# Kernel optimization log

Measured on AMD Instinct MI355X. Metric: run time of the kernel, lower is better.

## Reference

```python
import jax, jax.numpy as jnp
import numpy as np
import math

B, H, W, DM = 4, 64, 64, 96
DS, DCONV, EXPAND = 16, 3, 2
DI = EXPAND * DM
DTR = math.ceil(DM / 16)
K = 4
HID = 4 * DI


def layernorm(x, g, b, eps=1e-5):
    m = x.mean(-1, keepdims=True)
    v = ((x - m) ** 2).mean(-1, keepdims=True)
    return (x - m) / jnp.sqrt(v + eps) * g + b


def dwconv(x, w, b=None):
    # x: (B,C,H,W), w: (C,1,kh,kw) depthwise, odd kernel => SAME padding == k//2
    out = jax.lax.conv_general_dilated(x, w, (1, 1), 'SAME',
                                       feature_group_count=x.shape[1],
                                       dimension_numbers=('NCHW', 'OIHW', 'NCHW'))
    if b is not None:
        out = out + b[None, :, None, None]
    return out


def ss2d_core(xc, x_proj_w, dt_projs_w, dt_projs_b, A_logs, Ds):
    # xc: (b, d_inner, h, w) -> (b, d_inner, L) summed over 4 scan directions
    b, c, h, w = xc.shape
    L = h * w
    x_hw = xc.reshape(b, c, L)
    x_wh = xc.transpose(0, 1, 3, 2).reshape(b, c, L)
    xs = jnp.stack([x_hw, x_wh], axis=1)                 # (b,2,c,L)
    xs = jnp.concatenate([xs, jnp.flip(xs, -1)], axis=1)  # (b,4,c,L)
    x_dbl = jnp.einsum('bkdl,kcd->bkcl', xs, x_proj_w)
    dts, Bs, Cs = jnp.split(x_dbl, [DTR, DTR + DS], axis=2)
    dts = jnp.einsum('bkrl,kdr->bkdl', dts, dt_projs_w)
    delta = jax.nn.softplus(dts + dt_projs_b[None, :, :, None])  # (b,K,c,L)
    A = -jnp.exp(A_logs).reshape(K, c, DS)                       # (K,c,n)

    def step(hst, inp):
        x_t, d_t, B_t, C_t = inp  # (b,K,c),(b,K,c),(b,K,n),(b,K,n)
        dA = jnp.exp(d_t[..., None] * A)                       # (b,K,c,n)
        hst = hst * dA + (d_t * x_t)[..., None] * B_t[:, :, None, :]
        y = jnp.einsum('bkdn,bkn->bkd', hst, C_t)
        return hst, y

    seq = (jnp.moveaxis(xs, -1, 0), jnp.moveaxis(delta, -1, 0),
           jnp.moveaxis(Bs, -1, 0), jnp.moveaxis(Cs, -1, 0))
    h0 = jnp.zeros((b, K, c, DS), xc.dtype)
    _, ys = jax.lax.scan(step, h0, seq)          # (L,b,K,c)
    ys = jnp.moveaxis(ys, 0, -1)                 # (b,K,c,L)
    ys = ys + Ds.reshape(K, c)[None, :, :, None] * xs
    y1 = ys[:, 0]
    inv = jnp.flip(ys[:, 2:4], -1)
    y2 = inv[:, 0]
    wh = ys[:, 1].reshape(b, c, w, h).swapaxes(2, 3).reshape(b, c, L)
    invwh = inv[:, 1].reshape(b, c, w, h).swapaxes(2, 3).reshape(b, c, L)
    return y1 + y2 + wh + invwh


def msffn(y, in_w, in_b, dw1, dw3, dw5, ln_g, ln_b, out_w, out_b):
    hcl = jax.nn.silu(y @ in_w.T + in_b)          # (b,h,w,HID)
    hc = hcl.transpose(0, 3, 1, 2)
    hc = hc + dwconv(hc, dw1) + dwconv(hc, dw3) + dwconv(hc, dw5)
    hn = layernorm(hc.transpose(0, 2, 3, 1), ln_g, ln_b)
    return hn @ out_w.T + out_b


def setup_inputs() -> dict:
    key = jax.random.key(0)
    ks = jax.random.split(key, 16)
    dt_init_std = DTR ** -0.5
    dt = jnp.exp(jax.random.uniform(ks[0], (K, DI)) * (math.log(0.1) - math.log(0.001)) + math.log(0.001))
    dt = jnp.clip(dt, 1e-4, None)
    inv_dt = dt + jnp.log(-jnp.expm1(-dt))          # softplus-inverse init for dt bias
    A_logs = jnp.tile(jnp.log(jnp.arange(1, DS + 1, dtype=jnp.float32))[None, :], (K * DI, 1))
    r = lambda i, sh, s: jax.random.normal(ks[i], sh, jnp.float32) * s
    return {
        'x': r(1, (B, H, W, DM), 1.0),
        'in_proj_w': r(2, (2 * DI, DM), DM ** -0.5),
        'conv_w': r(3, (DI, 1, DCONV, DCONV), 0.2),
        'conv_b': jnp.zeros((DI,), jnp.float32),
        'x_proj_w': r(4, (K, DTR + 2 * DS, DI), DI ** -0.5),
        'dt_projs_w': jax.random.uniform(ks[5], (K, DI, DTR), minval=-dt_init_std, maxval=dt_init_std),
        'dt_projs_b': inv_dt,
        'A_logs': A_logs,
        'Ds': jnp.ones((K * DI,), jnp.float32),
        'out_norm_g': jnp.ones((DI,), jnp.float32),
        'out_norm_b': jnp.zeros((DI,), jnp.float32),
        'out_proj_w': r(6, (DM, DI), DI ** -0.5),
        'ffn_in_w': r(7, (HID, DI), DI ** -0.5),
        'ffn_in_b': jnp.zeros((HID,), jnp.float32),
        'ffn_dw1': r(8, (HID, 1, 1, 1), 0.3),
        'ffn_dw3': r(9, (HID, 1, 3, 3), 0.2),
        'ffn_dw5': r(10, (HID, 1, 5, 5), 0.1),
        'ffn_ln_g': jnp.ones((HID,), jnp.float32),
        'ffn_ln_b': jnp.zeros((HID,), jnp.float32),
        'ffn_out_w': r(11, (DM, HID), HID ** -0.5),
        'ffn_out_b': jnp.zeros((DM,), jnp.float32),
        'skip_scale': jnp.ones((1,), jnp.float32),
    }


def reference(x, in_proj_w, conv_w, conv_b, x_proj_w, dt_projs_w, dt_projs_b, A_logs, Ds,
              out_norm_g, out_norm_b, out_proj_w, ffn_in_w, ffn_in_b, ffn_dw1, ffn_dw3,
              ffn_dw5, ffn_ln_g, ffn_ln_b, ffn_out_w, ffn_out_b, skip_scale):
    b, h, w, _ = x.shape
    xz = x @ in_proj_w.T                          # (b,h,w,2*DI)
    xi, z = jnp.split(xz, 2, axis=-1)
    xc = jax.nn.silu(dwconv(xi.transpose(0, 3, 1, 2), conv_w, conv_b))  # (b,DI,h,w)
    y = ss2d_core(xc, x_proj_w, dt_projs_w, dt_projs_b, A_logs, Ds)     # (b,DI,L)
    y = y.swapaxes(1, 2).reshape(b, h, w, DI)
    y = layernorm(y, out_norm_g, out_norm_b)
    y = y * jax.nn.silu(z)
    out = y @ out_proj_w.T
    ffn = msffn(y, ffn_in_w, ffn_in_b, ffn_dw1, ffn_dw3, ffn_dw5,
                ffn_ln_g, ffn_ln_b, ffn_out_w, ffn_out_b)
    return out + skip_scale * ffn
```

## Files before the change

### kernel.cpp

```cpp
#include <hip/hip_runtime.h>
#include <hip/hip_bf16.h>

constexpr int BB = 4, HH = 64, WW = 64, DMv = 96;
constexpr int DSn = 16, DIv = 192, DTRv = 6, KKv = 4, HIDv = 768;
constexpr int LL = 4096;
constexpr int NC = 64, CHK = LL / NC;
constexpr int NR = BB * LL;
constexpr int XDS = 40;

constexpr size_t S_xi   = (size_t)BB * LL * DIv;
constexpr size_t S_xdbl = (size_t)BB * KKv * LL * XDS;
constexpr size_t S_big  = (size_t)BB * KKv * LL * DIv;
constexpr size_t S_sp   = (size_t)BB * KKv * NC * DIv * DSn;

typedef __attribute__((ext_vector_type(8))) short short8;
typedef __attribute__((ext_vector_type(4))) short short4v;
typedef __attribute__((ext_vector_type(4))) float floatx4;

__device__ __forceinline__ float sigf(float x) { return 1.f / (1.f + __expf(-x)); }
__device__ __forceinline__ float softp(float x) {
  return (x > 20.f) ? x : __logf(1.f + __expf(x));
}
__device__ __forceinline__ short bfbits(float v) {
  __hip_bfloat16 h = __float2bfloat16(v);
  return *(short*)&h;
}

__device__ __forceinline__ int lmap(int k, int l) {
  int lr = (k & 2) ? (LL - 1 - l) : l;
  return (k & 1) ? (((lr & 63) << 6) | (lr >> 6)) : lr;
}

__global__ void k_wprep(const float* __restrict__ fiw, const float* __restrict__ opw,
                        const float* __restrict__ fow, const float* __restrict__ in_w,
                        const float* __restrict__ xpw, const float* __restrict__ x,
                        float* __restrict__ wt, float* __restrict__ wcatT,
                        float* __restrict__ xt, short* __restrict__ fiwP,
                        short* __restrict__ opwP, short* __restrict__ fowP) {
  int bx = blockIdx.x, t = threadIdx.x;
  __shared__ float smbuf[32 * 65];
  if (bx < 36) {
    int r0 = (bx / 3) * 32, c0 = (bx % 3) * 32;
    float (*tile)[33] = (float(*)[33])smbuf;
    int tc = t & 31, tr = t >> 5;
#pragma unroll
    for (int i = 0; i < 4; ++i)
      tile[tr + i * 8][tc] = in_w[(size_t)(r0 + tr + i * 8) * 96 + c0 + tc];
    __syncthreads();
#pragma unroll
    for (int i = 0; i < 4; ++i)
      wt[(size_t)(c0 + tr + i * 8) * 384 + r0 + tc] = tile[tc][tr + i * 8];
    return;
  }
  if (bx < 150) {
    int idx = (bx - 36) * 256 + t;
    if (idx < 2 * 192 * 76) {
      int p = idx / (192 * 76);
      int rem = idx % (192 * 76);
      int d = rem / 76, j = rem % 76;
      int k = (j >= 38 ? 2 : 0) + p;
      int c = (j >= 38) ? j - 38 : j;
      wcatT[idx] = xpw[((size_t)(k * 38 + c)) * DIv + d];
    }
    return;
  }
  if (bx < 918) {
    int i4 = bx - 150;
    int r0 = (i4 / 3) * 64, k0 = (i4 % 3) * 32;
    float (*tile)[65] = (float(*)[65])smbuf;
#pragma unroll
    for (int ii = 0; ii < 8; ++ii) {
      int i = (t >> 5) + ii * 8, j = t & 31;
      tile[j][i] = x[(size_t)(r0 + i) * 96 + k0 + j];
    }
    __syncthreads();
#pragma unroll
    for (int jj = 0; jj < 8; ++jj) {
      int j = (t >> 6) + jj * 4, i = t & 63;
      xt[(size_t)(k0 + j) * NR + r0 + i] = tile[j][i];
    }
    return;
  }
  int lane = t & 63, ln16 = lane & 15, qd = lane >> 4;
  if (bx < 990) {
    int f = (bx - 918) * 4 + (t >> 6);
    int kt = f / 48, ntg = f % 48;
    int n = ntg * 16 + ln16;
#pragma unroll
    for (int j = 0; j < 8; ++j) {
      int k = kt * 32 + qd * 8 + j;
      fiwP[(size_t)f * 512 + lane * 8 + j] = bfbits(fiw[(size_t)n * DIv + k]);
    }
    return;
  }
  if (bx < 1008) {
    int u = (bx - 990) * 4 + (t >> 6);
    int f = u >> 1, part = u & 1;
    int kt = f / 6, ntg = f % 6;
    int n = ntg * 16 + ln16;
#pragma unroll
    for (int j = 0; j < 8; ++j) {
      int k = kt * 32 + qd * 8 + j;
      float w = opw[(size_t)n * DIv + k];
      __hip_bfloat16 h = __float2bfloat16(w);
      float v = part ? (w - (float)h) : w;
      opwP[((size_t)(part * 36 + f)) * 512 + lane * 8 + j] = bfbits(v);
    }
    return;
  }
  {
    int u = (bx - 1008) * 4 + (t >> 6);
    int f = u >> 1, part = u & 1;
    int kt = f / 6, ntg = f % 6;
    int n = ntg * 16 + ln16;
#pragma unroll
    for (int j = 0; j < 8; ++j) {
      int k = kt * 32 + qd * 8 + j;
      float w = fow[(size_t)n * HIDv + k];
      __hip_bfloat16 h = __float2bfloat16(w);
      float v = part ? (w - (float)h) : w;
      fowP[((size_t)(part * 144 + f)) * 512 + lane * 8 + j] = bfbits(v);
    }
  }
}

__global__ void k_inproj(const float* __restrict__ xt, const float* __restrict__ wt,
                         float* __restrict__ xi, float* __restrict__ z) {
  int t = threadIdx.x;
  int wv = t >> 6, lane = t & 63;
  int rq = blockIdx.x * 256 + wv * 64 + lane;
  int c0 = blockIdx.y * 8;
  const float4* xt4 = (const float4*)xt;
  float4 acc[8];
#pragma unroll
  for (int c = 0; c < 8; ++c) acc[c] = make_float4(0.f, 0.f, 0.f, 0.f);
  for (int k = 0; k < 96; ++k) {
    float4 xv = xt4[(size_t)k * (NR / 4) + rq];
    const float* wr = wt + k * 384 + c0;
#pragma unroll
    for (int c = 0; c < 8; ++c) {
      float w = wr[c];
      acc[c].x += w * xv.x; acc[c].y += w * xv.y;
      acc[c].z += w * xv.z; acc[c].w += w * xv.w;
    }
  }
  float* dst; int cc;
  if (c0 < DIv) { dst = xi; cc = c0; } else { dst = z; cc = c0 - DIv; }
#pragma unroll
  for (int li = 0; li < 4; ++li) {
    size_t row = (size_t)rq * 4 + li;
    float4 v0, v1;
    v0.x = (&acc[0].x)[li]; v0.y = (&acc[1].x)[li];
    v0.z = (&acc[2].x)[li]; v0.w = (&acc[3].x)[li];
    v1.x = (&acc[4].x)[li]; v1.y = (&acc[5].x)[li];
    v1.z = (&acc[6].x)[li]; v1.w = (&acc[7].x)[li];
    float4* o4 = (float4*)(dst + row * DIv + cc);
    o4[0] = v0; o4[1] = v1;
  }
}

constexpr int TW2 = 18;
__global__ void k_dwconv3(const float* __restrict__ xi, const float* __restrict__ cw,
                          const float* __restrict__ cb, float* __restrict__ xc,
                          float* __restrict__ xcT, float* __restrict__ xcTs) {
  int tile = blockIdx.x;
  int cg = blockIdx.y, b = blockIdx.z;
  int t = threadIdx.x;
  int ti0 = (tile >> 2) * 16, tj0 = (tile & 3) * 16;
  __shared__ float sm[TW2 * TW2 * 32];

  for (int e = t; e < TW2 * TW2 * 32; e += 256) {
    int ec = e & 31;
    int sp = e >> 5;
    int hi = sp / TW2, hj = sp % TW2;
    int gi = ti0 + hi - 1, gj = tj0 + hj - 1;
    float v = 0.f;
    if ((unsigned)gi < (unsigned)HH && (unsigned)gj < (unsigned)WW)
      v = xi[((size_t)b * LL + gi * WW + gj) * DIv + cg * 32 + ec];
    sm[e] = v;
  }

  int c = t & 31, s0 = t >> 5;
  int cglob = cg * 32 + c;
  float wc[9];
#pragma unroll
  for (int j = 0; j < 9; ++j) wc[j] = cw[cglob * 9 + j];
  float bv = cb[cglob];
  __syncthreads();

  float res[32];
  for (int i = 0; i < 32; ++i) {
    int p = s0 + (i << 3);
    int r = p >> 4, q = p & 15;
    float s = bv;
#pragma unroll
    for (int di = 0; di < 3; ++di)
#pragma unroll
      for (int dj = 0; dj < 3; ++dj)
        s += sm[((r + di) * TW2 + (q + dj)) * 32 + c] * wc[di * 3 + dj];
    res[i] = s * sigf(s);
  }
  __syncthreads();
  for (int i = 0; i < 32; ++i) {
    int p = s0 + (i << 3);
    sm[p * 35 + c] = res[i];
  }
  __syncthreads();
  for (int it = 0; it < 32; ++it) {
    int e = it * 256 + t;
    int p = e >> 5, ec = e & 31;
    int l = (ti0 + (p >> 4)) * WW + tj0 + (p & 15);
    xc[((size_t)b * LL + l) * DIv + cg * 32 + ec] = sm[p * 35 + ec];
  }
  for (int d2 = 0; d2 < 32; ++d2) {
    int l = (ti0 + (t >> 4)) * WW + tj0 + (t & 15);
    xcT[(size_t)(cg * 32 + d2) * NR + b * LL + l] = sm[t * 35 + d2];
  }
  for (int d2 = 0; d2 < 32; ++d2) {
    int gjo = t >> 4, gio = t & 15;
    int lt2 = (tj0 + gjo) * WW + ti0 + gio;
    int p = gio * 16 + gjo;
    xcTs[(size_t)(cg * 32 + d2) * NR + b * LL + lt2] = sm[p * 35 + d2];
  }
}

__global__ void k_xdbl2(const float* __restrict__ xcT, const float* __restrict__ xcTs,
                        const float* __restrict__ wcatT, float* __restrict__ xdbl) {
  int t = threadIdx.x;
  int rq = blockIdx.x * 256 + t;
  int jg = blockIdx.y;
  int pb = blockIdx.z;
  int p = pb >> 2, b = pb & 3;
  const float4* A = (const float4*)(p ? xcTs : xcT);
  const float* wbase = wcatT + (size_t)p * 192 * 76 + jg * 4;
  float4 acc[4];
#pragma unroll
  for (int j = 0; j < 4; ++j) acc[j] = make_float4(0.f, 0.f, 0.f, 0.f);
  for (int d = 0; d < 192; ++d) {
    float4 xv = A[(size_t)d * (NR / 4) + b * 1024 + rq];
    const float* wr = wbase + d * 76;
#pragma unroll
    for (int j = 0; j < 4; ++j) {
      float w = wr[j];
      acc[j].x += w * xv.x; acc[j].y += w * xv.y;
      acc[j].z += w * xv.z; acc[j].w += w * xv.w;
    }
  }
#pragma unroll
  for (int li = 0; li < 4; ++li) {
    int r = rq * 4 + li;
#pragma unroll
    for (int j = 0; j < 4; ++j) {
      int col = jg * 4 + j;
      int kk = (col >= 38) ? (2 + p) : p;
      int c = (col >= 38) ? col - 38 : col;
      int l = (col >= 38) ? (LL - 1 - r) : r;
      int phys = c + (c >= 6 ? 2 : 0);
      size_t ro = (((size_t)(b * KKv + kk)) * LL + l) * XDS;
      xdbl[ro + phys] = (&acc[j].x)[li];
      if (col == 5) { xdbl[ro + 6] = 0.f; xdbl[ro + 7] = 0.f; }
    }
  }
}

__global__ void k_scan1(const float* __restrict__ xdbl, const float* __restrict__ xc,
                        const float* __restrict__ alogs, const float* __restrict__ dtw,
                        const float* __restrict__ dtb,
                        float* __restrict__ S, float* __restrict__ P) {
  int bx = blockIdx.x;
  int c = bx / 3, dblk = bx % 3;
  int k = blockIdx.y, b = blockIdx.z;
  int t = threadIdx.x, dl = t >> 2, nq = t & 3;
  int d = dblk * 64 + dl;
  __shared__ float de_s[16][64], xv_s[16][64], bc_s[16][16];
  float A[4];
#pragma unroll
  for (int j = 0; j < 4; ++j)
    A[j] = -__expf(alogs[(size_t)(k * DIv + d) * DSn + nq * 4 + j]);
  int derow = t >> 4, dec0 = (t & 15) * 4;
  float DTW[4][6], DTB[4];
#pragma unroll
  for (int jj = 0; jj < 4; ++jj) {
    int dd = k * DIv + dblk * 64 + dec0 + jj;
    DTB[jj] = dtb[dd];
#pragma unroll
    for (int r2 = 0; r2 < 6; ++r2) DTW[jj][r2] = dtw[(size_t)dd * 6 + r2];
  }
  size_t bkL = (size_t)(b * KKv + k) * LL;
  const float* xq = xdbl + bkL * XDS;
  const float* xcb = xc + (size_t)b * LL * DIv;
  float h[4] = {0.f, 0.f, 0.f, 0.f}, sA[4] = {0.f, 0.f, 0.f, 0.f};
  int l0 = c * CHK;
  for (int tile = 0; tile < CHK / 16; ++tile) {
    int lt = l0 + tile * 16;
    __syncthreads();
    {
      int r = t >> 4, q = t & 15;
      int lc = lmap(k, lt + r);
      *(float4*)&xv_s[r][q * 4] = *(const float4*)(xcb + (size_t)lc * DIv + dblk * 64 + q * 4);
      if (t < 64) {
        int r2 = t >> 2, q2 = t & 3;
        *(float4*)&bc_s[r2][q2 * 4] = *(const float4*)(xq + (size_t)(lt + r2) * XDS + 8 + q2 * 4);
      }
      const float* dtp = xq + (size_t)(lt + derow) * XDS;
      float d0 = dtp[0], d1 = dtp[1], d2 = dtp[2], d3 = dtp[3], d4 = dtp[4], d5 = dtp[5];
#pragma unroll
      for (int jj = 0; jj < 4; ++jj) {
        float s = DTB[jj] + d0 * DTW[jj][0] + d1 * DTW[jj][1] + d2 * DTW[jj][2]
                          + d3 * DTW[jj][3] + d4 * DTW[jj][4] + d5 * DTW[jj][5];
        de_s[derow][dec0 + jj] = softp(s);
      }
    }
    __syncthreads();
#pragma unroll
    for (int i2 = 0; i2 < 16; ++i2) {
      float de = de_s[i2][dl];
      float xv = xv_s[i2][dl];
      float4 Bv = *(float4*)&bc_s[i2][nq * 4];
      float db = de * xv;
#pragma unroll
      for (int j = 0; j < 4; ++j) {
        float u = de * A[j];
        sA[j] += u;
        h[j] = h[j] * __expf(u) + db * (&Bv.x)[j];
      }
    }
  }
  size_t o = ((((size_t)(b * KKv + k) * NC + c) * 3 + dblk) * 1024) + (size_t)t * 4;
  float4 hs, ps;
#pragma unroll
  for (int j = 0; j < 4; ++j) { (&hs.x)[j] = h[j]; (&ps.x)[j] = __expf(sA[j]); }
  *(float4*)(S + o) = hs;
  *(float4*)(P + o) = ps;
}

__global__ void k_scan2(float* __restrict__ S, const float* __restrict__ P) {
  int dblk = blockIdx.x, k = blockIdx.y, b = blockIdx.z;
  int t = threadIdx.x;
  size_t base = (((size_t)(b * KKv + k) * NC) * 3 + dblk) * 1024 + (size_t)t * 4;
  float4 h = make_float4(0.f, 0.f, 0.f, 0.f);
  for (int c = 0; c < NC; ++c) {
    size_t o = base + (size_t)c * 3 * 1024;
    float4 s = *(float4*)(S + o), p = *(float4*)(P + o);
    *(float4*)(S + o) = h;
    h.x = s.x + p.x * h.x; h.y = s.y + p.y * h.y;
    h.z = s.z + p.z * h.z; h.w = s.w + p.w * h.w;
  }
}

__global__ void k_scan3(const float* __restrict__ xdbl, const float* __restrict__ xc,
                        const float* __restrict__ alogs, const float* __restrict__ dtw,
                        const float* __restrict__ dtb,
                        const float* __restrict__ Hin, float* __restrict__ ys) {
  int bx = blockIdx.x;
  int c = bx / 3, dblk = bx % 3;
  int k = blockIdx.y, b = blockIdx.z;
  int t = threadIdx.x, dl = t >> 2, nq = t & 3;
  int d = dblk * 64 + dl;
  __shared__ float de_s[16][64], xv_s[16][64], bc_s[16][32];
  float A[4];
#pragma unroll
  for (int j = 0; j < 4; ++j)
    A[j] = -__expf(alogs[(size_t)(k * DIv + d) * DSn + nq * 4 + j]);
  int derow = t >> 4, dec0 = (t & 15) * 4;
  float DTW[4][6], DTB[4];
#pragma unroll
  for (int jj = 0; jj < 4; ++jj) {
    int dd = k * DIv + dblk * 64 + dec0 + jj;
    DTB[jj] = dtb[dd];
#pragma unroll
    for (int r2 = 0; r2 < 6; ++r2) DTW[jj][r2] = dtw[(size_t)dd * 6 + r2];
  }
  size_t bkL = (size_t)(b * KKv + k) * LL;
  const float* xq = xdbl + bkL * XDS;
  const float* xcb = xc + (size_t)b * LL * DIv;
  float* yp = ys + bkL * DIv + d;
  size_t o = ((((size_t)(b * KKv + k) * NC + c) * 3 + dblk) * 1024) + (size_t)t * 4;
  float4 h4 = *(const float4*)(Hin + o);
  float h[4] = {h4.x, h4.y, h4.z, h4.w};
  int l0 = c * CHK;
  for (int tile = 0; tile < CHK / 16; ++tile) {
    int lt = l0 + tile * 16;
    __syncthreads();
    {
      int r = t >> 4, q = t & 15;
      int lc = lmap(k, lt + r);
      *(float4*)&xv_s[r][q * 4] = *(const float4*)(xcb + (size_t)lc * DIv + dblk * 64 + q * 4);
      if (t < 128) {
        int r2 = t >> 3, q2 = t & 7;
        *(float4*)&bc_s[r2][q2 * 4] = *(const float4*)(xq + (size_t)(lt + r2) * XDS + 8 + q2 * 4);
      }
      const float* dtp = xq + (size_t)(lt + derow) * XDS;
      float d0 = dtp[0], d1 = dtp[1], d2 = dtp[2], d3 = dtp[3], d4 = dtp[4], d5 = dtp[5];
#pragma unroll
      for (int jj = 0; jj < 4; ++jj) {
        float s = DTB[jj] + d0 * DTW[jj][0] + d1 * DTW[jj][1] + d2 * DTW[jj][2]
                          + d3 * DTW[jj][3] + d4 * DTW[jj][4] + d5 * DTW[jj][5];
        de_s[derow][dec0 + jj] = softp(s);
      }
    }
    __syncthreads();
#pragma unroll
    for (int i2 = 0; i2 < 16; ++i2) {
      float de = de_s[i2][dl];
      float xv = xv_s[i2][dl];
      float4 Bv = *(float4*)&bc_s[i2][nq * 4];
      float4 Cv = *(float4*)&bc_s[i2][16 + nq * 4];
      float db = de * xv;
      float p = 0.f;
#pragma unroll
      for (int j = 0; j < 4; ++j) {
        h[j] = h[j] * __expf(de * A[j]) + db * (&Bv.x)[j];
        p += h[j] * (&Cv.x)[j];
      }
      p += __shfl_down(p, 2, 4);
      p += __shfl_down(p, 1, 4);
      if (nq == 0) yp[(size_t)(lt + i2) * DIv] = p;
    }
  }
}

__global__ void k_comlnt(const float* __restrict__ ys, const float* __restrict__ xc,
                         const float* __restrict__ Ds, const float* __restrict__ z,
                         const float* __restrict__ g, const float* __restrict__ be,
                         __hip_bfloat16* __restrict__ ygtB,
                         __hip_bfloat16* __restrict__ ygtBl) {
  int bl0 = blockIdx.x * 32;
  int b = bl0 >> 12, l0 = bl0 & 4095;
  int t = threadIdx.x;
  __shared__ float vbuf[32 * 193];
  __shared__ float m_[32], rs_[32];
  {
    int grp = t >> 6, lane6 = t & 63;
    size_t base = (size_t)b * KKv * LL * DIv;
#pragma unroll
    for (int i8 = 0; i8 < 8; ++i8) {
      int li = grp + i8 * 4;
      int l = l0 + li;
      int lT = ((l & 63) << 6) | (l >> 6);
      const float* r0 = ys + base + (size_t)l * DIv;
      const float* r2 = ys + base + ((size_t)2 * LL + (LL - 1 - l)) * DIv;
      const float* r1 = ys + base + ((size_t)1 * LL + lT) * DIv;
      const float* r3 = ys + base + ((size_t)3 * LL + (LL - 1 - lT)) * DIv;
      const float* xr = xc + ((size_t)b * LL + l) * DIv;
#pragma unroll
      for (int cc = 0; cc < 3; ++cc) {
        int d = lane6 + cc * 64;
        float sd = Ds[d] + Ds[DIv + d] + Ds[2 * DIv + d] + Ds[3 * DIv + d];
        vbuf[li * 193 + d] = r0[d] + r2[d] + r1[d] + r3[d] + sd * xr[d];
      }
    }
  }
  __syncthreads();
  {
    int r = t >> 3, q = t & 7;
    float s = 0.f, qq = 0.f;
#pragma unroll
    for (int j = 0; j < 24; ++j) {
      float v = vbuf[r * 193 + q + j * 8];
      s += v; qq += v * v;
    }
    s += __shfl_down(s, 4, 8); qq += __shfl_down(qq, 4, 8);
    s += __shfl_down(s, 2, 8); qq += __shfl_down(qq, 2, 8);
    s += __shfl_down(s, 1, 8); qq += __shfl_down(qq, 1, 8);
    if (q == 0) {
      float m = s / DIv;
      m_[r] = m;
      rs_[r] = rsqrtf(qq / DIv - m * m + 1e-5f);
    }
  }
  __syncthreads();
  int tc = t & 31, tr = t >> 5;
#pragma unroll
  for (int ch = 0; ch < 6; ++ch) {
    int c0 = ch * 32;
    float gg = g[c0 + tc], bb = be[c0 + tc];
#pragma unroll
    for (int i = 0; i < 4; ++i) {
      int r = tr + i * 8;
      float v = vbuf[r * 193 + c0 + tc];
      float zz = z[(size_t)(bl0 + r) * DIv + c0 + tc];
      float val = (v - m_[r]) * rs_[r] * gg + bb;
      float gated = val * zz * sigf(zz);
      __hip_bfloat16 h = __float2bfloat16(gated);
      ygtB[(size_t)(bl0 + r) * DIv + c0 + tc] = h;
      ygtBl[(size_t)(bl0 + r) * DIv + c0 + tc] = __float2bfloat16(gated - (float)h);
    }
  }
}

__global__ void k_ffnmf(const __hip_bfloat16* __restrict__ ygtB,
                        const short* __restrict__ fiwP,
                        const float* __restrict__ bias, float* __restrict__ hcl) {
  int t = threadIdx.x;
  int wv = t >> 6, lane = t & 63;
  int ln16 = lane & 15, qd = lane >> 4;
  int m0 = blockIdx.x * 64 + wv * 16;
  int n0 = blockIdx.y * 64;
  int ntg0 = n0 >> 4;
  floatx4 acc[4];
  floatx4 zero4 = {0.f, 0.f, 0.f, 0.f};
// ... 75 lines not shown
#pragma unroll
      for (int dj = 0; dj < 5; ++dj)
        win[slot][dj] = sm[(((r + 4) * TW) + (q + dj)) * CG + c];
      float s = 0.f;
#pragma unroll
      for (int di = 0; di < 5; ++di) {
        int wsl = (r + di) % 5;
#pragma unroll
        for (int dj = 0; dj < 5; ++dj)
          s += win[wsl][dj] * wc[di * 5 + dj];
      }
      hc2[((size_t)b * LL + (ti0 + r) * WW + (tj0 + q)) * HIDv + cglob] = s;
    }
  }
}

constexpr int LNROWS = 16, LNPAD = 776;
__global__ void k_ln2b(const float* __restrict__ hc2, const float* __restrict__ g,
                       const float* __restrict__ be,
                       short* __restrict__ hnBh, short* __restrict__ hnBl) {
  int r0 = blockIdx.x * LNROWS;
  int t = threadIdx.x;
  __shared__ float rows[LNROWS * LNPAD];
  __shared__ float m_[LNROWS], rs_[LNROWS];
#pragma unroll
  for (int i = 0; i < 12; ++i) {
    int idx4 = t + i * 256;
    int row = idx4 / 192, c4 = idx4 % 192;
    float4 v = *(const float4*)(hc2 + (size_t)(r0 + row) * HIDv + c4 * 4);
    *(float4*)&rows[row * LNPAD + c4 * 4] = v;
  }
  __syncthreads();
  {
    int r = t >> 4, q = t & 15;
    float s = 0.f, qq = 0.f;
#pragma unroll
    for (int j = 0; j < 48; ++j) {
      float v = rows[r * LNPAD + q + j * 16];
      s += v; qq += v * v;
    }
    s += __shfl_down(s, 8, 16); qq += __shfl_down(qq, 8, 16);
    s += __shfl_down(s, 4, 16); qq += __shfl_down(qq, 4, 16);
    s += __shfl_down(s, 2, 16); qq += __shfl_down(qq, 2, 16);
    s += __shfl_down(s, 1, 16); qq += __shfl_down(qq, 1, 16);
    if (q == 0) {
      float m = s / HIDv;
      m_[r] = m;
      rs_[r] = rsqrtf(qq / HIDv - m * m + 1e-5f);
    }
  }
  __syncthreads();
#pragma unroll
  for (int i = 0; i < 12; ++i) {
    int idx4 = t + i * 256;
    int row = idx4 / 192, c4 = idx4 % 192;
    float4 v = *(const float4*)&rows[row * LNPAD + c4 * 4];
    float4 gv = *(const float4*)(g + c4 * 4);
    float4 bv = *(const float4*)(be + c4 * 4);
    float m = m_[row], rs = rs_[row];
    short4v hh, ll;
#pragma unroll
    for (int j = 0; j < 4; ++j) {
      float val = ((&v.x)[j] - m) * rs * (&gv.x)[j] + (&bv.x)[j];
      __hip_bfloat16 h = __float2bfloat16(val);
      hh[j] = *(short*)&h;
      ll[j] = bfbits(val - (float)h);
    }
    size_t o = (size_t)(r0 + row) * HIDv + c4 * 4;
    *(short4v*)(hnBh + o) = hh;
    *(short4v*)(hnBl + o) = ll;
  }
}

__global__ void k_finalmf(const short* __restrict__ hnBh, const short* __restrict__ hnBl,
                          const short* __restrict__ fowP,
                          const short* __restrict__ ygtBh, const short* __restrict__ ygtBl,
                          const short* __restrict__ opwP,
                          const float* __restrict__ fob, const float* __restrict__ skip,
                          float* __restrict__ dout) {
  int t = threadIdx.x;
  int wv = t >> 6, lane = t & 63;
  int ln16 = lane & 15, qd = lane >> 4;
  int m0 = blockIdx.x * 64 + wv * 16;
  int ntg0 = blockIdx.y * 3;
  floatx4 accF[3], accO[3];
  floatx4 zero4 = {0.f, 0.f, 0.f, 0.f};
#pragma unroll
  for (int nt = 0; nt < 3; ++nt) { accF[nt] = zero4; accO[nt] = zero4; }
  const short* arh = hnBh + (size_t)(m0 + ln16) * HIDv + qd * 8;
  const short* arl = hnBl + (size_t)(m0 + ln16) * HIDv + qd * 8;
#pragma unroll 4
  for (int kt = 0; kt < 24; ++kt) {
    short8 ah = *(const short8*)(arh + kt * 32);
    short8 al = *(const short8*)(arl + kt * 32);
    const short* bh = fowP + ((size_t)(kt * 6 + ntg0) * 64 + lane) * 8;
    const short* bl = fowP + ((size_t)(144 + kt * 6 + ntg0) * 64 + lane) * 8;
#pragma unroll
    for (int nt = 0; nt < 3; ++nt) {
      short8 bhv = *(const short8*)(bh + (size_t)nt * 512);
      short8 blv = *(const short8*)(bl + (size_t)nt * 512);
      accF[nt] = __builtin_amdgcn_mfma_f32_16x16x32_bf16(ah, bhv, accF[nt], 0, 0, 0);
      accF[nt] = __builtin_amdgcn_mfma_f32_16x16x32_bf16(al, bhv, accF[nt], 0, 0, 0);
      accF[nt] = __builtin_amdgcn_mfma_f32_16x16x32_bf16(ah, blv, accF[nt], 0, 0, 0);
    }
  }
  const short* orh = ygtBh + (size_t)(m0 + ln16) * DIv + qd * 8;
  const short* orl = ygtBl + (size_t)(m0 + ln16) * DIv + qd * 8;
#pragma unroll
  for (int kt = 0; kt < 6; ++kt) {
    short8 ah = *(const short8*)(orh + kt * 32);
    short8 al = *(const short8*)(orl + kt * 32);
    const short* bh = opwP + ((size_t)(kt * 6 + ntg0) * 64 + lane) * 8;
    const short* bl = opwP + ((size_t)(36 + kt * 6 + ntg0) * 64 + lane) * 8;
#pragma unroll
    for (int nt = 0; nt < 3; ++nt) {
      short8 bhv = *(const short8*)(bh + (size_t)nt * 512);
      short8 blv = *(const short8*)(bl + (size_t)nt * 512);
      accO[nt] = __builtin_amdgcn_mfma_f32_16x16x32_bf16(ah, bhv, accO[nt], 0, 0, 0);
      accO[nt] = __builtin_amdgcn_mfma_f32_16x16x32_bf16(al, bhv, accO[nt], 0, 0, 0);
      accO[nt] = __builtin_amdgcn_mfma_f32_16x16x32_bf16(ah, blv, accO[nt], 0, 0, 0);
    }
  }
  float sk = skip[0];
#pragma unroll
  for (int nt = 0; nt < 3; ++nt) {
    int col = (ntg0 + nt) * 16 + ln16;
    float bv = fob[col];
#pragma unroll
    for (int r = 0; r < 4; ++r) {
      int row = m0 + qd * 4 + r;
      dout[(size_t)row * DMv + col] = accO[nt][r] + sk * (accF[nt][r] + bv);
    }
  }
}

extern "C" void kernel_launch(void* const* d_in, const int* in_sizes, int n_in,
                              void* d_out, int out_size, void* d_ws, size_t ws_size,
                              hipStream_t stream) {
  const float* x        = (const float*)d_in[0];
  const float* in_w     = (const float*)d_in[1];
  const float* conv_w   = (const float*)d_in[2];
  const float* conv_b   = (const float*)d_in[3];
  const float* xpw      = (const float*)d_in[4];
  const float* dtw      = (const float*)d_in[5];
  const float* dtb      = (const float*)d_in[6];
  const float* alogs    = (const float*)d_in[7];
  const float* Ds       = (const float*)d_in[8];
  const float* ong      = (const float*)d_in[9];
  const float* onb      = (const float*)d_in[10];
  const float* opw      = (const float*)d_in[11];
  const float* fiw      = (const float*)d_in[12];
  const float* fib      = (const float*)d_in[13];
  const float* dw1      = (const float*)d_in[14];
  const float* dw3      = (const float*)d_in[15];
  const float* dw5      = (const float*)d_in[16];
  const float* flg      = (const float*)d_in[17];
  const float* flb      = (const float*)d_in[18];
  const float* fow      = (const float*)d_in[19];
  const float* fob      = (const float*)d_in[20];
  const float* skip     = (const float*)d_in[21];

  float* ws    = (float*)d_ws;
  float* xi    = ws;
  float* z     = xi + S_xi;
  float* xc    = z + S_xi;
  float* xdbl  = xc + S_xi;
  float* scr   = xdbl + S_xdbl;
  float* ys    = scr + S_big;
  float* wtiny = ys + S_big;
  float* wcatT = wtiny;
  float* wt    = wcatT + 29184;
  __hip_bfloat16* ygtB = (__hip_bfloat16*)(wt + 36864);
  short* fiwP  = (short*)(wt + 36864) + (size_t)NR * DIv;
  short* opwP  = fiwP + 288 * 512;
  short* fowP  = opwP + 2 * 36 * 512;

  float* xt = scr;
  k_wprep<<<1080, 256, 0, stream>>>(fiw, opw, fow, in_w, xpw, x,
                                    wt, wcatT, xt, fiwP, opwP, fowP);

  dim3 gip(NR / 1024, 48);
  k_inproj<<<gip, 256, 0, stream>>>(xt, wt, xi, z);

  float* xcT  = ys;
  float* xcTs = ys + S_xi;
  dim3 gdw(16, DIv / 32, BB);
  k_dwconv3<<<gdw, 256, 0, stream>>>(xi, conv_w, conv_b, xc, xcT, xcTs);

  dim3 gxd(4, 19, 8);
  k_xdbl2<<<gxd, 256, 0, stream>>>(xcT, xcTs, wcatT, xdbl);

  float* Sbuf = scr;
  float* Pbuf = scr + S_sp;
  dim3 gs13(NC * 3, KKv, BB);
  dim3 gs2(3, KKv, BB);
  k_scan1<<<gs13, 256, 0, stream>>>(xdbl, xc, alogs, dtw, dtb, Sbuf, Pbuf);
  k_scan2<<<gs2, 256, 0, stream>>>(Sbuf, Pbuf);
  k_scan3<<<gs13, 256, 0, stream>>>(xdbl, xc, alogs, dtw, dtb, Sbuf, ys);

  __hip_bfloat16* ygtBl = (__hip_bfloat16*)xi;
  k_comlnt<<<NR / 32, 256, 0, stream>>>(ys, xc, Ds, z, ong, onb, ygtB, ygtBl);

  float* hcl = scr;
  dim3 gmf(NR / 64, HIDv / 64);
  k_ffnmf<<<gmf, 256, 0, stream>>>(ygtB, fiwP, fib, hcl);

  float* hc2 = ys;
  dim3 gc(16, HIDv / CG, BB);
  k_ffnconv2<<<gc, 256, 0, stream>>>(hcl, dw1, dw3, dw5, hc2);

  short* hnBh = (short*)scr;
  short* hnBl = hnBh + (size_t)NR * HIDv;
  k_ln2b<<<NR / LNROWS, 256, 0, stream>>>(hc2, flg, flb, hnBh, hnBl);

  dim3 gfm(NR / 64, 2);
  k_finalmf<<<gfm, 256, 0, stream>>>(hnBh, hnBl, fowP,
                                     (const short*)ygtB, (const short*)ygtBl, opwP,
                                     fob, skip, (float*)d_out);
}
```

Baseline: 433.5 us.

## Move x_proj to split-bf16 MFMA, pipeline scan loads, widen final GEMM tiles

Replaces the scalar fp32 x_proj kernel with an MFMA kernel that uses hi/lo bf16 splits of both activations and weights. The depthwise conv now writes bf16 hi/lo copies instead of two transposed fp32 copies. The scan kernels halve the chunk count, prefetch the next tile into registers, compute delta per thread and share it by shuffle instead of through shared memory, and use exp2 with a pre-scaled A. The final GEMM has each block cover all 96 output columns rather than splitting them across two blocks. These changes touch several unrelated stages and trade launch parallelism and register pressure for less memory traffic and fewer synchronisations.

After: 426.9 us. About the same (-1.5%).

```diff
diff --git a/kernel.cpp b/kernel.cpp
--- a/kernel.cpp
+++ b/kernel.cpp
@@ -4,7 +4,7 @@
 constexpr int BB = 4, HH = 64, WW = 64, DMv = 96;
 constexpr int DSn = 16, DIv = 192, DTRv = 6, KKv = 4, HIDv = 768;
 constexpr int LL = 4096;
-constexpr int NC = 64, CHK = LL / NC;
+constexpr int NC = 32, CHK = LL / NC;
 constexpr int NR = BB * LL;
 constexpr int XDS = 40;
 
@@ -25,6 +25,13 @@
   __hip_bfloat16 h = __float2bfloat16(v);
   return *(short*)&h;
 }
+__device__ __forceinline__ float ex2(float x) {
+#if __has_builtin(__builtin_amdgcn_exp2f)
+  return __builtin_amdgcn_exp2f(x);
+#else
+  return exp2f(x);
+#endif
+}
 
 __device__ __forceinline__ int lmap(int k, int l) {
   int lr = (k & 2) ? (LL - 1 - l) : l;
@@ -34,9 +41,9 @@
 __global__ void k_wprep(const float* __restrict__ fiw, const float* __restrict__ opw,
                         const float* __restrict__ fow, const float* __restrict__ in_w,
                         const float* __restrict__ xpw, const float* __restrict__ x,
-                        float* __restrict__ wt, float* __restrict__ wcatT,
-                        float* __restrict__ xt, short* __restrict__ fiwP,
-                        short* __restrict__ opwP, short* __restrict__ fowP) {
+                        float* __restrict__ wt, float* __restrict__ xt,
+                        short* __restrict__ fiwP, short* __restrict__ opwP,
+                        short* __restrict__ fowP, short* __restrict__ wcatP) {
   int bx = blockIdx.x, t = threadIdx.x;
   __shared__ float smbuf[32 * 65];
   if (bx < 36) {
@@ -52,20 +59,8 @@
       wt[(size_t)(c0 + tr + i * 8) * 384 + r0 + tc] = tile[tc][tr + i * 8];
     return;
   }
-  if (bx < 150) {
-    int idx = (bx - 36) * 256 + t;
-    if (idx < 2 * 192 * 76) {
-      int p = idx / (192 * 76);
-      int rem = idx % (192 * 76);
-      int d = rem / 76, j = rem % 76;
-      int k = (j >= 38 ? 2 : 0) + p;
-      int c = (j >= 38) ? j - 38 : j;
-      wcatT[idx] = xpw[((size_t)(k * 38 + c)) * DIv + d];
-    }
-    return;
-  }
-  if (bx < 918) {
-    int i4 = bx - 150;
+  if (bx < 804) {
+    int i4 = bx - 36;
     int r0 = (i4 / 3) * 64, k0 = (i4 % 3) * 32;
     float (*tile)[65] = (float(*)[65])smbuf;
 #pragma unroll
@@ -82,8 +77,8 @@
     return;
   }
   int lane = t & 63, ln16 = lane & 15, qd = lane >> 4;
-  if (bx < 990) {
-    int f = (bx - 918) * 4 + (t >> 6);
+  if (bx < 876) {
+    int f = (bx - 804) * 4 + (t >> 6);
     int kt = f / 48, ntg = f % 48;
     int n = ntg * 16 + ln16;
 #pragma unroll
@@ -93,8 +88,8 @@
     }
     return;
   }
-  if (bx < 1008) {
-    int u = (bx - 990) * 4 + (t >> 6);
+  if (bx < 894) {
+    int u = (bx - 876) * 4 + (t >> 6);
     int f = u >> 1, part = u & 1;
     int kt = f / 6, ntg = f % 6;
     int n = ntg * 16 + ln16;
@@ -108,8 +103,8 @@
     }
     return;
   }
-  {
-    int u = (bx - 1008) * 4 + (t >> 6);
+  if (bx < 966) {
+    int u = (bx - 894) * 4 + (t >> 6);
     int f = u >> 1, part = u & 1;
     int kt = f / 6, ntg = f % 6;
     int n = ntg * 16 + ln16;
@@ -120,6 +115,27 @@
       __hip_bfloat16 h = __float2bfloat16(w);
       float v = part ? (w - (float)h) : w;
       fowP[((size_t)(part * 144 + f)) * 512 + lane * 8 + j] = bfbits(v);
+    }
+    return;
+  }
+  {
+    int u = (bx - 966) * 4 + (t >> 6);
+    int p = u / 60, r = u % 60;
+    int part = r / 30, r2 = r % 30;
+    int kt = r2 / 5, g = r2 % 5;
+    int n = g * 16 + ln16;
+#pragma unroll
+    for (int j = 0; j < 8; ++j) {
+      int kd = kt * 32 + qd * 8 + j;
+      float w = 0.f;
+      if (n < 76) {
+        int ksel = ((n >= 38) ? 2 : 0) + p;
+        int cc = (n >= 38) ? n - 38 : n;
+        w = xpw[(size_t)(ksel * 38 + cc) * DIv + kd];
+      }
+      __hip_bfloat16 h = __float2bfloat16(w);
+      float v = part ? (w - (float)h) : w;
+      wcatP[((size_t)(((p * 2 + part) * 6 + kt) * 5 + g)) * 512 + lane * 8 + j] = bfbits(v);
     }
   }
 }
@@ -162,7 +178,7 @@
 constexpr int TW2 = 18;
 __global__ void k_dwconv3(const float* __restrict__ xi, const float* __restrict__ cw,
                           const float* __restrict__ cb, float* __restrict__ xc,
-                          float* __restrict__ xcT, float* __restrict__ xcTs) {
+                          short* __restrict__ xcBh, short* __restrict__ xcBl) {
   int tile = blockIdx.x;
   int cg = blockIdx.y, b = blockIdx.z;
   int t = threadIdx.x;
@@ -210,55 +226,61 @@
     int e = it * 256 + t;
     int p = e >> 5, ec = e & 31;
     int l = (ti0 + (p >> 4)) * WW + tj0 + (p & 15);
-    xc[((size_t)b * LL + l) * DIv + cg * 32 + ec] = sm[p * 35 + ec];
-  }
-  for (int d2 = 0; d2 < 32; ++d2) {
-    int l = (ti0 + (t >> 4)) * WW + tj0 + (t & 15);
-    xcT[(size_t)(cg * 32 + d2) * NR + b * LL + l] = sm[t * 35 + d2];
-  }
-  for (int d2 = 0; d2 < 32; ++d2) {
-    int gjo = t >> 4, gio = t & 15;
-    int lt2 = (tj0 + gjo) * WW + ti0 + gio;
-    int p = gio * 16 + gjo;
-    xcTs[(size_t)(cg * 32 + d2) * NR + b * LL + lt2] = sm[p * 35 + d2];
-  }
-}
-
-__global__ void k_xdbl2(const float* __restrict__ xcT, const float* __restrict__ xcTs,
-                        const float* __restrict__ wcatT, float* __restrict__ xdbl) {
+    float v = sm[p * 35 + ec];
+    size_t idx = ((size_t)b * LL + l) * DIv + cg * 32 + ec;
+    xc[idx] = v;
+    __hip_bfloat16 hh = __float2bfloat16(v);
+    xcBh[idx] = *(short*)&hh;
+    xcBl[idx] = bfbits(v - (float)hh);
+  }
+}
+
+__global__ void k_xdblmf(const short* __restrict__ xcBh, const short* __restrict__ xcBl,
+                         const short* __restrict__ wcatP, float* __restrict__ xdbl) {
   int t = threadIdx.x;
-  int rq = blockIdx.x * 256 + t;
-  int jg = blockIdx.y;
-  int pb = blockIdx.z;
+  int wv = t >> 6, lane = t & 63;
+  int ln16 = lane & 15, qd = lane >> 4;
+  int pb = blockIdx.y;
   int p = pb >> 2, b = pb & 3;
-  const float4* A = (const float4*)(p ? xcTs : xcT);
-  const float* wbase = wcatT + (size_t)p * 192 * 76 + jg * 4;
-  float4 acc[4];
-#pragma unroll
-  for (int j = 0; j < 4; ++j) acc[j] = make_float4(0.f, 0.f, 0.f, 0.f);
-  for (int d = 0; d < 192; ++d) {
-    float4 xv = A[(size_t)d * (NR / 4) + b * 1024 + rq];
-    const float* wr = wbase + d * 76;
-#pragma unroll
-    for (int j = 0; j < 4; ++j) {
-      float w = wr[j];
-      acc[j].x += w * xv.x; acc[j].y += w * xv.y;
-      acc[j].z += w * xv.z; acc[j].w += w * xv.w;
-    }
-  }
-#pragma unroll
-  for (int li = 0; li < 4; ++li) {
-    int r = rq * 4 + li;
-#pragma unroll
-    for (int j = 0; j < 4; ++j) {
-      int col = jg * 4 + j;
-      int kk = (col >= 38) ? (2 + p) : p;
-      int c = (col >= 38) ? col - 38 : col;
-      int l = (col >= 38) ? (LL - 1 - r) : r;
-      int phys = c + (c >= 6 ? 2 : 0);
-      size_t ro = (((size_t)(b * KKv + kk)) * LL + l) * XDS;
-      xdbl[ro + phys] = (&acc[j].x)[li];
-      if (col == 5) { xdbl[ro + 6] = 0.f; xdbl[ro + 7] = 0.f; }
+  int m0 = blockIdx.x * 64 + wv * 16;
+  int r = m0 + ln16;
+  int l = p ? (((r & 63) << 6) | (r >> 6)) : r;
+  const short* ah = xcBh + ((size_t)(b * LL + l)) * DIv + qd * 8;
+  const short* al = xcBl + ((size_t)(b * LL + l)) * DIv + qd * 8;
+  floatx4 acc[5];
+  floatx4 zero4 = {0.f, 0.f, 0.f, 0.f};
+#pragma unroll
+  for (int g = 0; g < 5; ++g) acc[g] = zero4;
+#pragma unroll
+  for (int kt = 0; kt < 6; ++kt) {
+    short8 Ah = *(const short8*)(ah + kt * 32);
+    short8 Al = *(const short8*)(al + kt * 32);
+    const short* bh = wcatP + ((size_t)(((p * 2 + 0) * 6 + kt) * 5)) * 512 + lane * 8;
+    const short* bl = wcatP + ((size_t)(((p * 2 + 1) * 6 + kt) * 5)) * 512 + lane * 8;
+#pragma unroll
+    for (int g = 0; g < 5; ++g) {
+      short8 Bh = *(const short8*)(bh + (size_t)g * 512);
+      short8 Bl = *(const short8*)(bl + (size_t)g * 512);
+      acc[g] = __builtin_amdgcn_mfma_f32_16x16x32_bf16(Ah, Bh, acc[g], 0, 0, 0);
+      acc[g] = __builtin_amdgcn_mfma_f32_16x16x32_bf16(Al, Bh, acc[g], 0, 0, 0);
+      acc[g] = __builtin_amdgcn_mfma_f32_16x16x32_bf16(Ah, Bl, acc[g], 0, 0, 0);
+    }
+  }
+#pragma unroll
+  for (int g = 0; g < 5; ++g) {
+    int col = g * 16 + ln16;
+    if (col < 76) {
+#pragma unroll
+      for (int rr = 0; rr < 4; ++rr) {
+        int rowr = m0 + qd * 4 + rr;
+        int kk = (col >= 38) ? (2 + p) : p;
+        int cc = (col >= 38) ? col - 38 : col;
+        int lpos = (col >= 38) ? (LL - 1 - rowr) : rowr;
+        int phys = cc + (cc >= 6 ? 2 : 0);
+        size_t ro = (((size_t)(b * KKv + kk)) * LL + lpos) * XDS;
+        xdbl[ro + phys] = acc[g][rr];
+        if (col == 5) { xdbl[ro + 6] = 0.f; xdbl[ro + 7] = 0.f; }
+      }
     }
   }
 }
@@ -272,64 +294,67 @@
   int k = blockIdx.y, b = blockIdx.z;
   int t = threadIdx.x, dl = t >> 2, nq = t & 3;
   int d = dblk * 64 + dl;
-  __shared__ float de_s[16][64], xv_s[16][64], bc_s[16][16];
-  float A[4];
+  __shared__ float xv_s[16][64], bc_s[16][16], dt_s[16][8];
+  float A2[4];
 #pragma unroll
   for (int j = 0; j < 4; ++j)
-    A[j] = -__expf(alogs[(size_t)(k * DIv + d) * DSn + nq * 4 + j]);
-  int derow = t >> 4, dec0 = (t & 15) * 4;
-  float DTW[4][6], DTB[4];
-#pragma unroll
-  for (int jj = 0; jj < 4; ++jj) {
-    int dd = k * DIv + dblk * 64 + dec0 + jj;
-    DTB[jj] = dtb[dd];
-#pragma unroll
-    for (int r2 = 0; r2 < 6; ++r2) DTW[jj][r2] = dtw[(size_t)dd * 6 + r2];
-  }
+    A2[j] = -__expf(alogs[(size_t)(k * DIv + d) * DSn + nq * 4 + j]) * 1.44269504f;
+  float DTWr[6];
+  float DTBr = dtb[k * DIv + d];
+#pragma unroll
+  for (int r2 = 0; r2 < 6; ++r2) DTWr[r2] = dtw[(size_t)(k * DIv + d) * 6 + r2];
   size_t bkL = (size_t)(b * KKv + k) * LL;
   const float* xq = xdbl + bkL * XDS;
   const float* xcb = xc + (size_t)b * LL * DIv;
   float h[4] = {0.f, 0.f, 0.f, 0.f}, sA[4] = {0.f, 0.f, 0.f, 0.f};
   int l0 = c * CHK;
+  int sr = t >> 4, sq = t & 15;
+  float4 xvp, bcp, dtp;
+  {
+    int lc = lmap(k, l0 + sr);
+    xvp = *(const float4*)(xcb + (size_t)lc * DIv + dblk * 64 + sq * 4);
+    if (t < 64) bcp = *(const float4*)(xq + (size_t)(l0 + (t >> 2)) * XDS + 8 + (t & 3) * 4);
+    if (t < 32) dtp = *(const float4*)(xq + (size_t)(l0 + (t >> 1)) * XDS + (t & 1) * 4);
+  }
   for (int tile = 0; tile < CHK / 16; ++tile) {
-    int lt = l0 + tile * 16;
+    *(float4*)&xv_s[sr][sq * 4] = xvp;
+    if (t < 64) *(float4*)&bc_s[t >> 2][(t & 3) * 4] = bcp;
+    if (t < 32) *(float4*)&dt_s[t >> 1][(t & 1) * 4] = dtp;
     __syncthreads();
-    {
-      int r = t >> 4, q = t & 15;
-      int lc = lmap(k, lt + r);
-      *(float4*)&xv_s[r][q * 4] = *(const float4*)(xcb + (size_t)lc * DIv + dblk * 64 + q * 4);
-      if (t < 64) {
-        int r2 = t >> 2, q2 = t & 3;
-        *(float4*)&bc_s[r2][q2 * 4] = *(const float4*)(xq + (size_t)(lt + r2) * XDS + 8 + q2 * 4);
-      }
-      const float* dtp = xq + (size_t)(lt + derow) * XDS;
-      float d0 = dtp[0], d1 = dtp[1], d2 = dtp[2], d3 = dtp[3], d4 = dtp[4], d5 = dtp[5];
-#pragma unroll
-      for (int jj = 0; jj < 4; ++jj) {
-        float s = DTB[jj] + d0 * DTW[jj][0] + d1 * DTW[jj][1] + d2 * DTW[jj][2]
-                          + d3 * DTW[jj][3] + d4 * DTW[jj][4] + d5 * DTW[jj][5];
-        de_s[derow][dec0 + jj] = softp(s);
-      }
-    }
-    __syncthreads();
+    float de_local[4];
+#pragma unroll
+    for (int jj = 0; jj < 4; ++jj) {
+      const float* dr = dt_s[nq * 4 + jj];
+      float s = DTBr + dr[0] * DTWr[0] + dr[1] * DTWr[1] + dr[2] * DTWr[2]
+                     + dr[3] * DTWr[3] + dr[4] * DTWr[4] + dr[5] * DTWr[5];
+      de_local[jj] = softp(s);
+    }
+    if (tile + 1 < CHK / 16) {
+      int ln = l0 + (tile + 1) * 16;
+      int lc = lmap(k, ln + sr);
+      xvp = *(const float4*)(xcb + (size_t)lc * DIv + dblk * 64 + sq * 4);
+      if (t < 64) bcp = *(const float4*)(xq + (size_t)(ln + (t >> 2)) * XDS + 8 + (t & 3) * 4);
+      if (t < 32) dtp = *(const float4*)(xq + (size_t)(ln + (t >> 1)) * XDS + (t & 1) * 4);
+    }
 #pragma unroll
     for (int i2 = 0; i2 < 16; ++i2) {
-      float de = de_s[i2][dl];
+      float de = __shfl(de_local[i2 & 3], i2 >> 2, 4);
       float xv = xv_s[i2][dl];
       float4 Bv = *(float4*)&bc_s[i2][nq * 4];
       float db = de * xv;
 #pragma unroll
       for (int j = 0; j < 4; ++j) {
-        float u = de * A[j];
+        float u = de * A2[j];
         sA[j] += u;
-        h[j] = h[j] * __expf(u) + db * (&Bv.x)[j];
+        h[j] = h[j] * ex2(u) + db * (&Bv.x)[j];
       }
     }
+    __syncthreads();
   }
   size_t o = ((((size_t)(b * KKv + k) * NC + c) * 3 + dblk) * 1024) + (size_t)t * 4;
   float4 hs, ps;
 #pragma unroll
-  for (int j = 0; j < 4; ++j) { (&hs.x)[j] = h[j]; (&ps.x)[j] = __expf(sA[j]); }
+  for (int j = 0; j < 4; ++j) { (&hs.x)[j] = h[j]; (&ps.x)[j] = ex2(sA[j]); }
   *(float4*)(S + o) = hs;
   *(float4*)(P + o) = ps;
 }
@@ -357,20 +382,15 @@
   int k = blockIdx.y, b = blockIdx.z;
   int t = threadIdx.x, dl = t >> 2, nq = t & 3;
   int d = dblk * 64 + dl;
-  __shared__ float de_s[16][64], xv_s[16][64], bc_s[16][32];
-  float A[4];
+  __shared__ float xv_s[16][64], bc_s[16][32], dt_s[16][8];
+  float A2[4];
 #pragma unroll
   for (int j = 0; j < 4; ++j)
-    A[j] = -__expf(alogs[(size_t)(k * DIv + d) * DSn + nq * 4 + j]);
-  int derow = t >> 4, dec0 = (t & 15) * 4;
-  float DTW[4][6], DTB[4];
-#pragma unroll
-  for (int jj = 0; jj < 4; ++jj) {
-    int dd = k * DIv + dblk * 64 + dec0 + jj;
-    DTB[jj] = dtb[dd];
-#pragma unroll
-    for (int r2 = 0; r2 < 6; ++r2) DTW[jj][r2] = dtw[(size_t)dd * 6 + r2];
-  }
+    A2[j] = -__expf(alogs[(size_t)(k * DIv + d) * DSn + nq * 4 + j]) * 1.44269504f;
+  float DTWr[6];
+  float DTBr = dtb[k * DIv + d];
+#pragma unroll
+  for (int r2 = 0; r2 < 6; ++r2) DTWr[r2] = dtw[(size_t)(k * DIv + d) * 6 + r2];
   size_t bkL = (size_t)(b * KKv + k) * LL;
   const float* xq = xdbl + bkL * XDS;
   const float* xcb = xc + (size_t)b * LL * DIv;
@@ -379,30 +399,38 @@
   float4 h4 = *(const float4*)(Hin + o);
   float h[4] = {h4.x, h4.y, h4.z, h4.w};
   int l0 = c * CHK;
+  int sr = t >> 4, sq = t & 15;
+  float4 xvp, bcp, dtp;
+  {
+    int lc = lmap(k, l0 + sr);
+    xvp = *(const float4*)(xcb + (size_t)lc * DIv + dblk * 64 + sq * 4);
+    if (t < 128) bcp = *(const float4*)(xq + (size_t)(l0 + (t >> 3)) * XDS + 8 + (t & 7) * 4);
+    if (t < 32) dtp = *(const float4*)(xq + (size_t)(l0 + (t >> 1)) * XDS + (t & 1) * 4);
+  }
   for (int tile = 0; tile < CHK / 16; ++tile) {
     int lt = l0 + tile * 16;
+    *(float4*)&xv_s[sr][sq * 4] = xvp;
+    if (t < 128) *(float4*)&bc_s[t >> 3][(t & 7) * 4] = bcp;
+    if (t < 32) *(float4*)&dt_s[t >> 1][(t & 1) * 4] = dtp;
     __syncthreads();
-    {
-      int r = t >> 4, q = t & 15;
-      int lc = lmap(k, lt + r);
-      *(float4*)&xv_s[r][q * 4] = *(const float4*)(xcb + (size_t)lc * DIv + dblk * 64 + q * 4);
-      if (t < 128) {
-        int r2 = t >> 3, q2 = t & 7;
-        *(float4*)&bc_s[r2][q2 * 4] = *(const float4*)(xq + (size_t)(lt + r2) * XDS + 8 + q2 * 4);
-      }
-      const float* dtp = xq + (size_t)(lt + derow) * XDS;
-      float d0 = dtp[0], d1 = dtp[1], d2 = dtp[2], d3 = dtp[3], d4 = dtp[4], d5 = dtp[5];
-#pragma unroll
-      for (int jj = 0; jj < 4; ++jj) {
-        float s = DTB[jj] + d0 * DTW[jj][0] + d1 * DTW[jj][1] + d2 * DTW[jj][2]
-                          + d3 * DTW[jj][3] + d4 * DTW[jj][4] + d5 * DTW[jj][5];
-        de_s[derow][dec0 + jj] = softp(s);
-      }
-    }
-    __syncthreads();
+    float de_local[4];
+#pragma unroll
+    for (int jj = 0; jj < 4; ++jj) {
+      const float* dr = dt_s[nq * 4 + jj];
+      float s = DTBr + dr[0] * DTWr[0] + dr[1] * DTWr[1] + dr[2] * DTWr[2]
+                     + dr[3] * DTWr[3] + dr[4] * DTWr[4] + dr[5] * DTWr[5];
+      de_local[jj] = softp(s);
+    }
+    if (tile + 1 < CHK / 16) {
+      int ln = l0 + (tile + 1) * 16;
+      int lc = lmap(k, ln + sr);
+      xvp = *(const float4*)(xcb + (size_t)lc * DIv + dblk * 64 + sq * 4);
+      if (t < 128) bcp = *(const float4*)(xq + (size_t)(ln + (t >> 3)) * XDS + 8 + (t & 7) * 4);
+      if (t < 32) dtp = *(const float4*)(xq + (size_t)(ln + (t >> 1)) * XDS + (t & 1) * 4);
+    }
 #pragma unroll
     for (int i2 = 0; i2 < 16; ++i2) {
-      float de = de_s[i2][dl];
+      float de = __shfl(de_local[i2 & 3], i2 >> 2, 4);
       float xv = xv_s[i2][dl];
       float4 Bv = *(float4*)&bc_s[i2][nq * 4];
       float4 Cv = *(float4*)&bc_s[i2][16 + nq * 4];
@@ -410,13 +438,14 @@
       float p = 0.f;
 #pragma unroll
       for (int j = 0; j < 4; ++j) {
-        h[j] = h[j] * __expf(de * A[j]) + db * (&Bv.x)[j];
+        h[j] = h[j] * ex2(de * A2[j]) + db * (&Bv.x)[j];
         p += h[j] * (&Cv.x)[j];
       }
       p += __shfl_down(p, 2, 4);
       p += __shfl_down(p, 1, 4);
       if (nq == 0) yp[(size_t)(lt + i2) * DIv] = p;
     }
+    __syncthreads();
   }
 }
 
@@ -658,21 +687,20 @@
   int wv = t >> 6, lane = t & 63;
   int ln16 = lane & 15, qd = lane >> 4;
   int m0 = blockIdx.x * 64 + wv * 16;
-  int ntg0 = blockIdx.y * 3;
-  floatx4 accF[3], accO[3];
+  floatx4 accF[6], accO[6];
   floatx4 zero4 = {0.f, 0.f, 0.f, 0.f};
 #pragma unroll
-  for (int nt = 0; nt < 3; ++nt) { accF[nt] = zero4; accO[nt] = zero4; }
+  for (int nt = 0; nt < 6; ++nt) { accF[nt] = zero4; accO[nt] = zero4; }
   const short* arh = hnBh + (size_t)(m0 + ln16) * HIDv + qd * 8;
   const short* arl = hnBl + (size_t)(m0 + ln16) * HIDv + qd * 8;
-#pragma unroll 4
+#pragma unroll 2
   for (int kt = 0; kt < 24; ++kt) {
     short8 ah = *(const short8*)(arh + kt * 32);
     short8 al = *(const short8*)(arl + kt * 32);
-    const short* bh = fowP + ((size_t)(kt * 6 + ntg0) * 64 + lane) * 8;
-    const short* bl = fowP + ((size_t)(144 + kt * 6 + ntg0) * 64 + lane) * 8;
-#pragma unroll
-    for (int nt = 0; nt < 3; ++nt) {
+    const short* bh = fowP + ((size_t)(kt * 6) * 64 + lane) * 8;
+    const short* bl = fowP + ((size_t)(144 + kt * 6) * 64 + lane) * 8;
+#pragma unroll
+    for (int nt = 0; nt < 6; ++nt) {
       short8 bhv = *(const short8*)(bh + (size_t)nt * 512);
       short8 blv = *(const short8*)(bl + (size_t)nt * 512);
       accF[nt] = __builtin_amdgcn_mfma_f32_16x16x32_bf16(ah, bhv, accF[nt], 0, 0, 0);
@@ -682,14 +710,14 @@
   }
   const short* orh = ygtBh + (size_t)(m0 + ln16) * DIv + qd * 8;
   const short* orl = ygtBl + (size_t)(m0 + ln16) * DIv + qd * 8;
-#pragma unroll
+#pragma unroll 2
   for (int kt = 0; kt < 6; ++kt) {
     short8 ah = *(const short8*)(orh + kt * 32);
     short8 al = *(const short8*)(orl + kt * 32);
-    const short* bh = opwP + ((size_t)(kt * 6 + ntg0) * 64 + lane) * 8;
-    const short* bl = opwP + ((size_t)(36 + kt * 6 + ntg0) * 64 + lane) * 8;
-#pragma unroll
-    for (int nt = 0; nt < 3; ++nt) {
+    const short* bh = opwP + ((size_t)(kt * 6) * 64 + lane) * 8;
+    const short* bl = opwP + ((size_t)(36 + kt * 6) * 64 + lane) * 8;
+#pragma unroll
+    for (int nt = 0; nt < 6; ++nt) {
       short8 bhv = *(const short8*)(bh + (size_t)nt * 512);
       short8 blv = *(const short8*)(bl + (size_t)nt * 512);
       accO[nt] = __builtin_amdgcn_mfma_f32_16x16x32_bf16(ah, bhv, accO[nt], 0, 0, 0);
@@ -699,8 +727,8 @@
   }
   float sk = skip[0];
 #pragma unroll
-  for (int nt = 0; nt < 3; ++nt) {
-    int col = (ntg0 + nt) * 16 + ln16;
+  for (int nt = 0; nt < 6; ++nt) {
+    int col = nt * 16 + ln16;
     float bv = fob[col];
 #pragma unroll
     for (int r = 0; r < 4; ++r) {
@@ -744,27 +772,27 @@
   float* scr   = xdbl + S_xdbl;
   float* ys    = scr + S_big;
   float* wtiny = ys + S_big;
-  float* wcatT = wtiny;
-  float* wt    = wcatT + 29184;
+  float* wt    = wtiny;
   __hip_bfloat16* ygtB = (__hip_bfloat16*)(wt + 36864);
   short* fiwP  = (short*)(wt + 36864) + (size_t)NR * DIv;
   short* opwP  = fiwP + 288 * 512;
   short* fowP  = opwP + 2 * 36 * 512;
+  short* wcatP = fowP + 2 * 144 * 512;
 
   float* xt = scr;
-  k_wprep<<<1080, 256, 0, stream>>>(fiw, opw, fow, in_w, xpw, x,
-                                    wt, wcatT, xt, fiwP, opwP, fowP);
+  k_wprep<<<996, 256, 0, stream>>>(fiw, opw, fow, in_w, xpw, x,
+                                   wt, xt, fiwP, opwP, fowP, wcatP);
 
   dim3 gip(NR / 1024, 48);
   k_inproj<<<gip, 256, 0, stream>>>(xt, wt, xi, z);
 
-  float* xcT  = ys;
-  float* xcTs = ys + S_xi;
+  short* xcBh = (short*)ys;
+  short* xcBl = xcBh + (size_t)NR * DIv;
   dim3 gdw(16, DIv / 32, BB);
-  k_dwconv3<<<gdw, 256, 0, stream>>>(xi, conv_w, conv_b, xc, xcT, xcTs);
-
-  dim3 gxd(4, 19, 8);
-  k_xdbl2<<<gxd, 256, 0, stream>>>(xcT, xcTs, wcatT, xdbl);
+  k_dwconv3<<<gdw, 256, 0, stream>>>(xi, conv_w, conv_b, xc, xcBh, xcBl);
+
+  dim3 gxd(LL / 64, 8);
+  k_xdblmf<<<gxd, 256, 0, stream>>>(xcBh, xcBl, wcatP, xdbl);
 
   float* Sbuf = scr;
   float* Pbuf = scr + S_sp;
@@ -789,8 +817,7 @@
   short* hnBl = hnBh + (size_t)NR * HIDv;
   k_ln2b<<<NR / LNROWS, 256, 0, stream>>>(hc2, flg, flb, hnBh, hnBl);
 
-  dim3 gfm(NR / 64, 2);
-  k_finalmf<<<gfm, 256, 0, stream>>>(hnBh, hnBl, fowP,
-                                     (const short*)ygtB, (const short*)ygtBl, opwP,
-                                     fob, skip, (float*)d_out);
-}
+  k_finalmf<<<NR / 64, 256, 0, stream>>>(hnBh, hnBl, fowP,
+                                         (const short*)ygtB, (const short*)ygtBl, opwP,
+                                         fob, skip, (float*)d_out);
+}
```
